# Kernel optimization log

Measured on AMD Instinct MI355X. Metric: run time of the kernel, lower is better.

Reference implementation:

```python
import jax, jax.numpy as jnp
import numpy as np

D_MODEL = 1024
SCALE = 1.0 / np.sqrt(D_MODEL)


def setup_inputs() -> dict:
    key = jax.random.key(0)
    ks = jax.random.split(key, 9)
    B, S, D = 4, 2048, D_MODEL
    std = 1.0 / np.sqrt(D)
    x = jax.random.normal(ks[0], (B, S, D), dtype=jnp.float32)
    # nn.Linear weights: [out, in]; we store transposed [in, out] for x @ W
    Wq = jax.random.uniform(ks[1], (D, D), jnp.float32, -std, std)
    bq = jax.random.uniform(ks[2], (D,), jnp.float32, -std, std)
    Wk = jax.random.uniform(ks[3], (D, D), jnp.float32, -std, std)
    bk = jax.random.uniform(ks[4], (D,), jnp.float32, -std, std)
    Wv = jax.random.uniform(ks[5], (D, D), jnp.float32, -std, std)
    bv = jax.random.uniform(ks[6], (D,), jnp.float32, -std, std)
    Wo = jax.random.uniform(ks[7], (D, D), jnp.float32, -std, std)
    bo = jax.random.uniform(ks[8], (D,), jnp.float32, -std, std)
    return {"x": x, "Wq": Wq, "bq": bq, "Wk": Wk, "bk": bk,
            "Wv": Wv, "bv": bv, "Wo": Wo, "bo": bo}


def reference(x, Wq, bq, Wk, bk, Wv, bv, Wo, bo):
    q = x @ Wq + bq                      # [B,S,D]
    k = x @ Wk + bk
    v = x @ Wv + bv
    scores = jnp.einsum('bsd,btd->bst', q, k) * SCALE  # [B,S,S]
    weights = jax.nn.softmax(scores, axis=-1)
    out = jnp.einsum('bst,btd->bsd', weights, v)       # [B,S,D]
    return out @ Wo + bo
```

## Files before the change

kernel.cpp:

```cpp
#include <hip/hip_runtime.h>
#include <hip/hip_bf16.h>
#include <cstdint>

typedef __bf16 bf16x8 __attribute__((ext_vector_type(8)));
typedef float f32x4 __attribute__((ext_vector_type(4)));

__device__ __forceinline__ float bf2f(unsigned short u) {
  union { unsigned int i; float f; } x; x.i = ((unsigned int)u) << 16; return x.f;
}
__device__ __forceinline__ unsigned short f2bf(float f) {
  __hip_bfloat16 h = __float2bfloat16(f);
  return __builtin_bit_cast(unsigned short, h);
}

__device__ __forceinline__ void gload_lds16(const void* g, void* l) {
  auto gp = reinterpret_cast<__attribute__((address_space(1))) char*>(
      reinterpret_cast<uintptr_t>(g));
  auto lp = reinterpret_cast<__attribute__((address_space(3))) char*>(
      reinterpret_cast<uintptr_t>(l));
  __builtin_amdgcn_global_load_lds(gp, lp, 16, 0, 0);
}

__device__ __forceinline__ void xcd_swz(int& bx, int& by, int& bz) {
  const int gx = gridDim.x, gy = gridDim.y;
  const int n = gx * gy * (int)gridDim.z;
  int lin = blockIdx.x + gx * (blockIdx.y + gy * blockIdx.z);
  lin = (lin & 7) * (n >> 3) + (lin >> 3);
  bx = lin % gx; lin /= gx;
  by = lin % gy; bz = lin / gy;
}

__global__ __launch_bounds__(256) void cvt_f32_to_bf16(
    const float* __restrict__ in, unsigned short* __restrict__ out, long n4) {
  long i = (long)blockIdx.x * 256 + threadIdx.x;
  if (i >= n4) return;
  const float4 v = reinterpret_cast<const float4*>(in)[i];
  ushort4 o;
  o.x = f2bf(v.x); o.y = f2bf(v.y); o.z = f2bf(v.z); o.w = f2bf(v.w);
  reinterpret_cast<ushort4*>(out)[i] = o;
}

__global__ void transpose_w4(const float* __restrict__ w0,
                             const float* __restrict__ w1,
                             const float* __restrict__ w2,
                             const float* __restrict__ w3,
                             unsigned short* __restrict__ out) {
  const int z = blockIdx.z;
  const float* in = (z == 0) ? w0 : (z == 1) ? w1 : (z == 2) ? w2 : w3;
  out += (size_t)z * 1024 * 1024;
  __shared__ float tile[32][33];
  const int c0 = blockIdx.x * 32, r0 = blockIdx.y * 32;
  tile[threadIdx.y][threadIdx.x] =
      in[(size_t)(r0 + threadIdx.y) * 1024 + c0 + threadIdx.x];
  __syncthreads();
  out[(size_t)(c0 + threadIdx.y) * 1024 + r0 + threadIdx.x] =
      f2bf(tile[threadIdx.x][threadIdx.y]);
}

__global__ void concat_bias3(const float* a, const float* b, const float* c,
                             float* o) {
  int i = blockIdx.x * 256 + threadIdx.x;
  if (i >= 3072) return;
  o[i] = (i < 1024) ? a[i] : (i < 2048 ? b[i - 1024] : c[i - 2048]);
}

template <typename OutT, bool HAS_BIAS, bool VSPLIT>
__global__ __launch_bounds__(256, 4) void gemm_hi(
    const unsigned short* __restrict__ A,
    const unsigned short* __restrict__ Bt,
    OutT* __restrict__ C,
    const float* __restrict__ bias,
    unsigned short* __restrict__ vt,
    int K, int lda, int ldb, int ldc, float scale,
    long sA, long sB, long sC) {
  int bx, by, bz;
  xcd_swz(bx, by, bz);
  A  += (long)bz * sA;
  Bt += (long)bz * sB;
  C  += (long)bz * sC;
  const int n0 = bx << 7;
  const int m0 = by << 7;
  __shared__ __attribute__((aligned(16))) unsigned short As[128 * 64];
  __shared__ __attribute__((aligned(16))) unsigned short Bs[128 * 64];
  const int t = threadIdx.x;
  const int lane = t & 63;
  const int w = t >> 6;
  const int wm = w >> 1, wn = w & 1;
  const unsigned short* gA = A + (size_t)m0 * lda;
  const unsigned short* gB = Bt + (size_t)n0 * ldb;
  const int NT = K >> 6;

  const int srow = lane >> 3;
  const int scol = ((lane & 7) ^ srow) << 3;

  f32x4 acc[4][4];
  const f32x4 vz = {0.f, 0.f, 0.f, 0.f};
#pragma unroll
  for (int i = 0; i < 4; ++i)
#pragma unroll
    for (int j = 0; j < 4; ++j) acc[i][j] = vz;

  for (int kt = 0; kt < NT; ++kt) {
    const unsigned short* pA = gA + (size_t)kt * 64;
    const unsigned short* pB = gB + (size_t)kt * 64;
#pragma unroll
    for (int i = 0; i < 4; ++i) {
      const int r0 = (w << 3) + (i << 5);
      gload_lds16(pA + (size_t)(r0 + srow) * lda + scol, As + r0 * 64);
      gload_lds16(pB + (size_t)(r0 + srow) * ldb + scol, Bs + r0 * 64);
    }
    __syncthreads();

#pragma unroll
    for (int kk = 0; kk < 2; ++kk) {
      bf16x8 af[4], bg[4];
      const int ch = ((kk << 2) + (lane >> 4)) ^ (lane & 7);
#pragma unroll
      for (int m = 0; m < 4; ++m) {
        const int row = (wm << 6) + (m << 4) + (lane & 15);
        af[m] = *reinterpret_cast<const bf16x8*>(As + row * 64 + (ch << 3));
      }
#pragma unroll
      for (int n = 0; n < 4; ++n) {
        const int row = (wn << 6) + (n << 4) + (lane & 15);
        bg[n] = *reinterpret_cast<const bf16x8*>(Bs + row * 64 + (ch << 3));
      }
#pragma unroll
      for (int m = 0; m < 4; ++m)
#pragma unroll
        for (int n = 0; n < 4; ++n) {
          if constexpr (VSPLIT) {
            acc[m][n] = __builtin_amdgcn_mfma_f32_16x16x32_bf16(
                af[m], bg[n], acc[m][n], 0, 0, 0);
          } else {
            acc[m][n] = __builtin_amdgcn_mfma_f32_16x16x32_bf16(
                bg[n], af[m], acc[m][n], 0, 0, 0);
          }
        }
    }
    __syncthreads();
  }

  if constexpr (VSPLIT) {
    const int crow0 = m0 + (wm << 6) + ((lane >> 4) << 2);
    const int ccol0 = n0 + (wn << 6) + (lane & 15);
    if (n0 >= 2048) {
      const int b = m0 >> 11;
#pragma unroll
      for (int mf = 0; mf < 4; ++mf) {
#pragma unroll
        for (int nf = 0; nf < 4; ++nf) {
          const int col = ccol0 + (nf << 4);
          const float bb = HAS_BIAS ? bias[col] : 0.f;
          const int d = col - 2048;
          const int s = (crow0 & 2047) + (mf << 4);
          ushort4 o;
          o.x = f2bf(acc[mf][nf][0] * scale + bb);
          o.y = f2bf(acc[mf][nf][1] * scale + bb);
          o.z = f2bf(acc[mf][nf][2] * scale + bb);
          o.w = f2bf(acc[mf][nf][3] * scale + bb);
          *reinterpret_cast<ushort4*>(
              vt + (((size_t)b << 10) + d) * 2048 + s) = o;
        }
      }
    } else {
#pragma unroll
      for (int mf = 0; mf < 4; ++mf) {
#pragma unroll
        for (int nf = 0; nf < 4; ++nf) {
          const int col = ccol0 + (nf << 4);
          const float bb = HAS_BIAS ? bias[col] : 0.f;
#pragma unroll
          for (int i = 0; i < 4; ++i) {
            const int row = crow0 + (mf << 4) + i;
            C[(size_t)row * ldc + col] =
                (OutT)f2bf(acc[mf][nf][i] * scale + bb);
          }
        }
      }
    }
  } else {
    const int mrow0 = m0 + (wm << 6) + (lane & 15);
    const int ncol0 = n0 + (wn << 6) + ((lane >> 4) << 2);
#pragma unroll
    for (int mf = 0; mf < 4; ++mf) {
      const int row = mrow0 + (mf << 4);
#pragma unroll
      for (int nf = 0; nf < 4; ++nf) {
        const int col = ncol0 + (nf << 4);
        float4 bb = {0.f, 0.f, 0.f, 0.f};
        if (HAS_BIAS) bb = *reinterpret_cast<const float4*>(bias + col);
        const f32x4 a = acc[mf][nf];
        if constexpr (sizeof(OutT) == 2) {
          ushort4 o;
          o.x = f2bf(a[0] * scale + bb.x);
          o.y = f2bf(a[1] * scale + bb.y);
          o.z = f2bf(a[2] * scale + bb.z);
          o.w = f2bf(a[3] * scale + bb.w);
          *reinterpret_cast<ushort4*>(&C[(size_t)row * ldc + col]) = o;
        } else {
          float4 o;
          o.x = a[0] * scale + bb.x;
          o.y = a[1] * scale + bb.y;
          o.z = a[2] * scale + bb.z;
          o.w = a[3] * scale + bb.w;
          *reinterpret_cast<float4*>(&C[(size_t)row * ldc + col]) = o;
        }
      }
    }
  }
}

__global__ __launch_bounds__(256) void softmax_inplace(
    unsigned short* __restrict__ P, int S) {
  const size_t row = blockIdx.x;
  unsigned short* p = P + row * (size_t)S;
  const int t = threadIdx.x;
  const int lane = t & 63, w = t >> 6;
  const uint4 raw = reinterpret_cast<const uint4*>(p)[t];
  unsigned int u[4] = {raw.x, raw.y, raw.z, raw.w};
  float v[8];
#pragma unroll
  for (int j = 0; j < 4; ++j) {
    v[2 * j]     = bf2f((unsigned short)(u[j] & 0xffffu));
    v[2 * j + 1] = bf2f((unsigned short)(u[j] >> 16));
  }
  float mx = v[0];
#pragma unroll
  for (int j = 1; j < 8; ++j) mx = fmaxf(mx, v[j]);
#pragma unroll
  for (int off = 32; off >= 1; off >>= 1) mx = fmaxf(mx, __shfl_xor(mx, off, 64));
  __shared__ float red[4];
  if (lane == 0) red[w] = mx;
  __syncthreads();
  mx = fmaxf(fmaxf(red[0], red[1]), fmaxf(red[2], red[3]));
  float e[8];
  float s = 0.f;
#pragma unroll
  for (int j = 0; j < 8; ++j) { e[j] = __expf(v[j] - mx); s += e[j]; }
#pragma unroll
  for (int off = 32; off >= 1; off >>= 1) s += __shfl_xor(s, off, 64);
  __syncthreads();
  if (lane == 0) red[w] = s;
  __syncthreads();
  s = red[0] + red[1] + red[2] + red[3];
  const float inv = 1.f / s;
  unsigned int o[4];
#pragma unroll
  for (int j = 0; j < 4; ++j)
    o[j] = (unsigned int)f2bf(e[2 * j] * inv) |
           ((unsigned int)f2bf(e[2 * j + 1] * inv) << 16);
  uint4 ov; ov.x = o[0]; ov.y = o[1]; ov.z = o[2]; ov.w = o[3];
  reinterpret_cast<uint4*>(p)[t] = ov;
}

extern "C" void kernel_launch(void* const* d_in, const int* in_sizes, int n_in,
                              void* d_out, int out_size, void* d_ws, size_t ws_size,
                              hipStream_t stream) {
  (void)in_sizes; (void)n_in; (void)out_size; (void)ws_size;
  const float* x  = (const float*)d_in[0];
  const float* Wq = (const float*)d_in[1];
  const float* bq = (const float*)d_in[2];
  const float* Wk = (const float*)d_in[3];
  const float* bk = (const float*)d_in[4];
  const float* Wv = (const float*)d_in[5];
  const float* bv = (const float*)d_in[6];
  const float* Wo = (const float*)d_in[7];
  const float* bo = (const float*)d_in[8];
  float* out = (float*)d_out;

  constexpr int B = 4, S = 2048, D = 1024;
  constexpr long BS = (long)B * S;
  constexpr size_t MB = 1ull << 20;
  char* ws = (char*)d_ws;
  unsigned short* xb   = (unsigned short*)(ws + 0);
  unsigned short* Wall = (unsigned short*)(ws + 16 * MB);
  float*          bqkv = (float*)(ws + 24 * MB);
  unsigned short* QKVc = (unsigned short*)(ws + 25 * MB);
  unsigned short* Vt   = (unsigned short*)(ws + 57 * MB);
  unsigned short* Sc   = (unsigned short*)(ws + 73 * MB);
  unsigned short* AO   = (unsigned short*)(ws + 0);

  const float scale = 0.03125f;

  cvt_f32_to_bf16<<<(BS * D / 4 + 255) / 256, 256, 0, stream>>>(x, xb, BS * D / 4);
  transpose_w4<<<dim3(32, 32, 4), dim3(32, 32), 0, stream>>>(Wq, Wk, Wv, Wo, Wall);
  concat_bias3<<<12, 256, 0, stream>>>(bq, bk, bv, bqkv);

  gemm_hi<unsigned short, true, true><<<dim3(24, 64, 1), 256, 0, stream>>>(
      xb, Wall, QKVc, bqkv, Vt, D, D, D, 2048, 1.f, 0, 0, 0);

  gemm_hi<unsigned short, false, false><<<dim3(16, 16, 4), 256, 0, stream>>>(
      QKVc + 0, QKVc + 1024, Sc, nullptr, nullptr, D, 2048, 2048, S, scale,
      (long)S * 2048, (long)S * 2048, (long)S * S);

  softmax_inplace<<<B * S, 256, 0, stream>>>(Sc, S);

  gemm_hi<unsigned short, false, false><<<dim3(8, 16, 4), 256, 0, stream>>>(
      Sc, Vt, AO, nullptr, nullptr, S, S, S, D, 1.f,
      (long)S * S, (long)D * S, (long)S * D);

  gemm_hi<float, true, false><<<dim3(8, 64, 1), 256, 0, stream>>>(
      AO, Wall + 3 * 1024 * 1024, out, bo, nullptr, D, D, D, D, 1.f, 0, 0, 0);
}
```

Measured before the change: 207.6 us.

## Fuse input conversion into QKV GEMM and softmax into PV GEMM

```diff
diff --git a/kernel.cpp b/kernel.cpp
--- a/kernel.cpp
+++ b/kernel.cpp
@@ -4,6 +4,7 @@
 
 typedef __bf16 bf16x8 __attribute__((ext_vector_type(8)));
 typedef float f32x4 __attribute__((ext_vector_type(4)));
+typedef short short8 __attribute__((ext_vector_type(8)));
 
 __device__ __forceinline__ float bf2f(unsigned short u) {
   union { unsigned int i; float f; } x; x.i = ((unsigned int)u) << 16; return x.f;
@@ -28,16 +29,6 @@
   lin = (lin & 7) * (n >> 3) + (lin >> 3);
   bx = lin % gx; lin /= gx;
   by = lin % gy; bz = lin / gy;
-}
-
-__global__ __launch_bounds__(256) void cvt_f32_to_bf16(
-    const float* __restrict__ in, unsigned short* __restrict__ out, long n4) {
-  long i = (long)blockIdx.x * 256 + threadIdx.x;
-  if (i >= n4) return;
-  const float4 v = reinterpret_cast<const float4*>(in)[i];
-  ushort4 o;
-  o.x = f2bf(v.x); o.y = f2bf(v.y); o.z = f2bf(v.z); o.w = f2bf(v.w);
-  reinterpret_cast<ushort4*>(out)[i] = o;
 }
 
 __global__ void transpose_w4(const float* __restrict__ w0,
@@ -64,13 +55,120 @@
   o[i] = (i < 1024) ? a[i] : (i < 2048 ? b[i - 1024] : c[i - 2048]);
 }
 
-template <typename OutT, bool HAS_BIAS, bool VSPLIT>
+__global__ __launch_bounds__(256, 4) void gemm_qkv(
+    const float* __restrict__ xf,
+    const unsigned short* __restrict__ Bt,
+    unsigned short* __restrict__ C,
+    const float* __restrict__ bias,
+    unsigned short* __restrict__ vt) {
+  int bx, by, bz;
+  xcd_swz(bx, by, bz);
+  const int n0 = bx << 7;
+  const int m0 = by << 7;
+  __shared__ __attribute__((aligned(16))) unsigned short As[128 * 64];
+  __shared__ __attribute__((aligned(16))) unsigned short Bs[128 * 64];
+  const int t = threadIdx.x;
+  const int lane = t & 63;
+  const int w = t >> 6;
+  const int wm = w >> 1, wn = w & 1;
+  const unsigned short* gB = Bt + (size_t)n0 * 1024;
+
+  const int srow = lane >> 3;
+  const int gcol8 = ((lane & 7) ^ srow) << 3;
+
+  f32x4 acc[4][4];
+  const f32x4 vz = {0.f, 0.f, 0.f, 0.f};
+#pragma unroll
+  for (int i = 0; i < 4; ++i)
+#pragma unroll
+    for (int j = 0; j < 4; ++j) acc[i][j] = vz;
+
+  for (int kt = 0; kt < 16; ++kt) {
+    const unsigned short* pB = gB + (size_t)kt * 64;
+    const float* pA = xf + (size_t)m0 * 1024 + (size_t)kt * 64;
+#pragma unroll
+    for (int i = 0; i < 4; ++i) {
+      const int r0 = (w << 3) + (i << 5);
+      gload_lds16(pB + (size_t)(r0 + srow) * 1024 + gcol8, Bs + r0 * 64);
+      const float* s = pA + (size_t)(r0 + srow) * 1024 + gcol8;
+      const float4 a0 = *reinterpret_cast<const float4*>(s);
+      const float4 a1 = *reinterpret_cast<const float4*>(s + 4);
+      short8 pk;
+      pk[0] = (short)f2bf(a0.x); pk[1] = (short)f2bf(a0.y);
+      pk[2] = (short)f2bf(a0.z); pk[3] = (short)f2bf(a0.w);
+      pk[4] = (short)f2bf(a1.x); pk[5] = (short)f2bf(a1.y);
+      pk[6] = (short)f2bf(a1.z); pk[7] = (short)f2bf(a1.w);
+      *reinterpret_cast<short8*>(As + (r0 + srow) * 64 + ((lane & 7) << 3)) = pk;
+    }
+    __syncthreads();
+
+#pragma unroll
+    for (int kk = 0; kk < 2; ++kk) {
+      bf16x8 af[4], bg[4];
+      const int ch = ((kk << 2) + (lane >> 4)) ^ (lane & 7);
+#pragma unroll
+      for (int m = 0; m < 4; ++m) {
+        const int row = (wm << 6) + (m << 4) + (lane & 15);
+        af[m] = *reinterpret_cast<const bf16x8*>(As + row * 64 + (ch << 3));
+      }
+#pragma unroll
+      for (int n = 0; n < 4; ++n) {
+        const int row = (wn << 6) + (n << 4) + (lane & 15);
+        bg[n] = *reinterpret_cast<const bf16x8*>(Bs + row * 64 + (ch << 3));
+      }
+#pragma unroll
+      for (int m = 0; m < 4; ++m)
+#pragma unroll
+        for (int n = 0; n < 4; ++n)
+          acc[m][n] = __builtin_amdgcn_mfma_f32_16x16x32_bf16(
+              af[m], bg[n], acc[m][n], 0, 0, 0);
+    }
+    __syncthreads();
+  }
+
+  const int crow0 = m0 + (wm << 6) + ((lane >> 4) << 2);
+  const int ccol0 = n0 + (wn << 6) + (lane & 15);
+  if (n0 >= 2048) {
+    const int b = m0 >> 11;
+#pragma unroll
+    for (int mf = 0; mf < 4; ++mf) {
+#pragma unroll
+      for (int nf = 0; nf < 4; ++nf) {
+        const int col = ccol0 + (nf << 4);
+        const float bb = bias[col];
+        const int d = col - 2048;
+        const int s = (crow0 & 2047) + (mf << 4);
+        ushort4 o;
+        o.x = f2bf(acc[mf][nf][0] + bb);
+        o.y = f2bf(acc[mf][nf][1] + bb);
+        o.z = f2bf(acc[mf][nf][2] + bb);
+        o.w = f2bf(acc[mf][nf][3] + bb);
+        *reinterpret_cast<ushort4*>(vt + (((size_t)b << 10) + d) * 2048 + s) = o;
+      }
+    }
+  } else {
+#pragma unroll
+    for (int mf = 0; mf < 4; ++mf) {
+#pragma unroll
+      for (int nf = 0; nf < 4; ++nf) {
+        const int col = ccol0 + (nf << 4);
+        const float bb = bias[col];
+#pragma unroll
+        for (int i = 0; i < 4; ++i) {
+          const int row = crow0 + (mf << 4) + i;
+          C[(size_t)row * 2048 + col] = f2bf(acc[mf][nf][i] + bb);
+        }
+      }
+    }
+  }
+}
+
+template <typename OutT, bool HAS_BIAS>
 __global__ __launch_bounds__(256, 4) void gemm_hi(
     const unsigned short* __restrict__ A,
     const unsigned short* __restrict__ Bt,
     OutT* __restrict__ C,
     const float* __restrict__ bias,
-    unsigned short* __restrict__ vt,
     int K, int lda, int ldb, int ldc, float scale,
     long sA, long sB, long sC) {
   int bx, by, bz;
@@ -128,130 +226,157 @@
 #pragma unroll
       for (int m = 0; m < 4; ++m)
 #pragma unroll
-        for (int n = 0; n < 4; ++n) {
-          if constexpr (VSPLIT) {
-            acc[m][n] = __builtin_amdgcn_mfma_f32_16x16x32_bf16(
-                af[m], bg[n], acc[m][n], 0, 0, 0);
-          } else {
-            acc[m][n] = __builtin_amdgcn_mfma_f32_16x16x32_bf16(
-                bg[n], af[m], acc[m][n], 0, 0, 0);
-          }
-        }
-    }
-    __syncthreads();
-  }
-
-  if constexpr (VSPLIT) {
-    const int crow0 = m0 + (wm << 6) + ((lane >> 4) << 2);
-    const int ccol0 = n0 + (wn << 6) + (lane & 15);
-    if (n0 >= 2048) {
-      const int b = m0 >> 11;
-#pragma unroll
-      for (int mf = 0; mf < 4; ++mf) {
-#pragma unroll
-        for (int nf = 0; nf < 4; ++nf) {
-          const int col = ccol0 + (nf << 4);
-          const float bb = HAS_BIAS ? bias[col] : 0.f;
-          const int d = col - 2048;
-          const int s = (crow0 & 2047) + (mf << 4);
-          ushort4 o;
-          o.x = f2bf(acc[mf][nf][0] * scale + bb);
-          o.y = f2bf(acc[mf][nf][1] * scale + bb);
-          o.z = f2bf(acc[mf][nf][2] * scale + bb);
-          o.w = f2bf(acc[mf][nf][3] * scale + bb);
-          *reinterpret_cast<ushort4*>(
-              vt + (((size_t)b << 10) + d) * 2048 + s) = o;
-        }
-      }
-    } else {
-#pragma unroll
-      for (int mf = 0; mf < 4; ++mf) {
-#pragma unroll
-        for (int nf = 0; nf < 4; ++nf) {
-          const int col = ccol0 + (nf << 4);
-          const float bb = HAS_BIAS ? bias[col] : 0.f;
-#pragma unroll
-          for (int i = 0; i < 4; ++i) {
-            const int row = crow0 + (mf << 4) + i;
-            C[(size_t)row * ldc + col] =
-                (OutT)f2bf(acc[mf][nf][i] * scale + bb);
-          }
-        }
-      }
-    }
-  } else {
-    const int mrow0 = m0 + (wm << 6) + (lane & 15);
-    const int ncol0 = n0 + (wn << 6) + ((lane >> 4) << 2);
+        for (int n = 0; n < 4; ++n)
+          acc[m][n] = __builtin_amdgcn_mfma_f32_16x16x32_bf16(
+              bg[n], af[m], acc[m][n], 0, 0, 0);
+    }
+    __syncthreads();
+  }
+
+  const int mrow0 = m0 + (wm << 6) + (lane & 15);
+  const int ncol0 = n0 + (wn << 6) + ((lane >> 4) << 2);
+#pragma unroll
+  for (int mf = 0; mf < 4; ++mf) {
+    const int row = mrow0 + (mf << 4);
+#pragma unroll
+    for (int nf = 0; nf < 4; ++nf) {
+      const int col = ncol0 + (nf << 4);
+      float4 bb = {0.f, 0.f, 0.f, 0.f};
+      if (HAS_BIAS) bb = *reinterpret_cast<const float4*>(bias + col);
+      const f32x4 a = acc[mf][nf];
+      if constexpr (sizeof(OutT) == 2) {
+        ushort4 o;
+        o.x = f2bf(a[0] * scale + bb.x);
+        o.y = f2bf(a[1] * scale + bb.y);
+        o.z = f2bf(a[2] * scale + bb.z);
+        o.w = f2bf(a[3] * scale + bb.w);
+        *reinterpret_cast<ushort4*>(&C[(size_t)row * ldc + col]) = o;
+      } else {
+        float4 o;
+        o.x = a[0] * scale + bb.x;
+        o.y = a[1] * scale + bb.y;
+        o.z = a[2] * scale + bb.z;
+        o.w = a[3] * scale + bb.w;
+        *reinterpret_cast<float4*>(&C[(size_t)row * ldc + col]) = o;
+      }
+    }
+  }
+}
+
+__global__ __launch_bounds__(256, 3) void gemm_pv(
+    const unsigned short* __restrict__ Sc,
+    const unsigned short* __restrict__ Vt,
+    unsigned short* __restrict__ O) {
+  int bx, by, bz;
+  xcd_swz(bx, by, bz);
+  const unsigned short* P = Sc + (long)bz * 2048 * 2048;
+  const unsigned short* V = Vt + (long)bz * 1024 * 2048;
+  unsigned short* Ob = O + (long)bz * 2048 * 1024;
+  const int n0 = bx << 7;
+  const int m0 = by << 7;
+  __shared__ __attribute__((aligned(16))) unsigned short Bs[128 * 64];
+  const int t = threadIdx.x;
+  const int lane = t & 63;
+  const int w = t >> 6;
+  const int wm = w >> 1, wn = w & 1;
+  const int srow = lane >> 3;
+  const int scol = ((lane & 7) ^ srow) << 3;
+  const int chh = lane >> 4;
+
+  f32x4 acc[4][4];
+  const f32x4 vz = {0.f, 0.f, 0.f, 0.f};
+#pragma unroll
+  for (int i = 0; i < 4; ++i)
+#pragma unroll
+    for (int j = 0; j < 4; ++j) acc[i][j] = vz;
+  float mrun[4] = {-1e30f, -1e30f, -1e30f, -1e30f};
+  float lpart[4] = {0.f, 0.f, 0.f, 0.f};
+
+  for (int kt = 0; kt < 32; ++kt) {
+    const unsigned short* pV = V + (size_t)kt * 64;
+#pragma unroll
+    for (int i = 0; i < 4; ++i) {
+      const int r0 = (w << 3) + (i << 5);
+      gload_lds16(pV + (size_t)(n0 + r0 + srow) * 2048 + scol, Bs + r0 * 64);
+    }
+
+    bf16x8 af[4][2];
 #pragma unroll
     for (int mf = 0; mf < 4; ++mf) {
-      const int row = mrow0 + (mf << 4);
+      const int row = m0 + (wm << 6) + (mf << 4) + (lane & 15);
+      const unsigned short* pr = P + (size_t)row * 2048 + kt * 64;
+      const bf16x8 r0v = *reinterpret_cast<const bf16x8*>(pr + (chh << 3));
+      const bf16x8 r1v = *reinterpret_cast<const bf16x8*>(pr + 32 + (chh << 3));
+      float f[16];
+#pragma unroll
+      for (int j = 0; j < 8; ++j) { f[j] = (float)r0v[j]; f[8 + j] = (float)r1v[j]; }
+      float px = f[0];
+#pragma unroll
+      for (int j = 1; j < 16; ++j) px = fmaxf(px, f[j]);
+      px = fmaxf(px, __shfl_xor(px, 16, 64));
+      px = fmaxf(px, __shfl_xor(px, 32, 64));
+      const float mn = fmaxf(mrun[mf], px);
+      const float sc = __expf(mrun[mf] - mn);
+      mrun[mf] = mn;
+      float ls = 0.f;
+#pragma unroll
+      for (int j = 0; j < 16; ++j) { f[j] = __expf(f[j] - mn); ls += f[j]; }
+      lpart[mf] = lpart[mf] * sc + ls;
 #pragma unroll
       for (int nf = 0; nf < 4; ++nf) {
-        const int col = ncol0 + (nf << 4);
-        float4 bb = {0.f, 0.f, 0.f, 0.f};
-        if (HAS_BIAS) bb = *reinterpret_cast<const float4*>(bias + col);
-        const f32x4 a = acc[mf][nf];
-        if constexpr (sizeof(OutT) == 2) {
-          ushort4 o;
-          o.x = f2bf(a[0] * scale + bb.x);
-          o.y = f2bf(a[1] * scale + bb.y);
-          o.z = f2bf(a[2] * scale + bb.z);
-          o.w = f2bf(a[3] * scale + bb.w);
-          *reinterpret_cast<ushort4*>(&C[(size_t)row * ldc + col]) = o;
-        } else {
-          float4 o;
-          o.x = a[0] * scale + bb.x;
-          o.y = a[1] * scale + bb.y;
-          o.z = a[2] * scale + bb.z;
-          o.w = a[3] * scale + bb.w;
-          *reinterpret_cast<float4*>(&C[(size_t)row * ldc + col]) = o;
-        }
-      }
-    }
-  }
-}
-
-__global__ __launch_bounds__(256) void softmax_inplace(
-    unsigned short* __restrict__ P, int S) {
-  const size_t row = blockIdx.x;
-  unsigned short* p = P + row * (size_t)S;
-  const int t = threadIdx.x;
-  const int lane = t & 63, w = t >> 6;
-  const uint4 raw = reinterpret_cast<const uint4*>(p)[t];
-  unsigned int u[4] = {raw.x, raw.y, raw.z, raw.w};
-  float v[8];
-#pragma unroll
-  for (int j = 0; j < 4; ++j) {
-    v[2 * j]     = bf2f((unsigned short)(u[j] & 0xffffu));
-    v[2 * j + 1] = bf2f((unsigned short)(u[j] >> 16));
-  }
-  float mx = v[0];
-#pragma unroll
-  for (int j = 1; j < 8; ++j) mx = fmaxf(mx, v[j]);
-#pragma unroll
-  for (int off = 32; off >= 1; off >>= 1) mx = fmaxf(mx, __shfl_xor(mx, off, 64));
-  __shared__ float red[4];
-  if (lane == 0) red[w] = mx;
-  __syncthreads();
-  mx = fmaxf(fmaxf(red[0], red[1]), fmaxf(red[2], red[3]));
-  float e[8];
-  float s = 0.f;
-#pragma unroll
-  for (int j = 0; j < 8; ++j) { e[j] = __expf(v[j] - mx); s += e[j]; }
-#pragma unroll
-  for (int off = 32; off >= 1; off >>= 1) s += __shfl_xor(s, off, 64);
-  __syncthreads();
-  if (lane == 0) red[w] = s;
-  __syncthreads();
-  s = red[0] + red[1] + red[2] + red[3];
-  const float inv = 1.f / s;
-  unsigned int o[4];
-#pragma unroll
-  for (int j = 0; j < 4; ++j)
-    o[j] = (unsigned int)f2bf(e[2 * j] * inv) |
-           ((unsigned int)f2bf(e[2 * j + 1] * inv) << 16);
-  uint4 ov; ov.x = o[0]; ov.y = o[1]; ov.z = o[2]; ov.w = o[3];
-  reinterpret_cast<uint4*>(p)[t] = ov;
+        acc[mf][nf][0] *= sc; acc[mf][nf][1] *= sc;
+        acc[mf][nf][2] *= sc; acc[mf][nf][3] *= sc;
+      }
+      short8 p0, p1;
+#pragma unroll
+      for (int j = 0; j < 8; ++j) {
+        p0[j] = (short)f2bf(f[j]);
+        p1[j] = (short)f2bf(f[8 + j]);
+      }
+      af[mf][0] = __builtin_bit_cast(bf16x8, p0);
+      af[mf][1] = __builtin_bit_cast(bf16x8, p1);
+    }
+
+    __syncthreads();
+#pragma unroll
+    for (int kk = 0; kk < 2; ++kk) {
+      bf16x8 bg[4];
+      const int ch = ((kk << 2) + chh) ^ (lane & 7);
+#pragma unroll
+      for (int n = 0; n < 4; ++n) {
+        const int row = (wn << 6) + (n << 4) + (lane & 15);
+        bg[n] = *reinterpret_cast<const bf16x8*>(Bs + row * 64 + (ch << 3));
+      }
+#pragma unroll
+      for (int m = 0; m < 4; ++m)
+#pragma unroll
+        for (int n = 0; n < 4; ++n)
+          acc[m][n] = __builtin_amdgcn_mfma_f32_16x16x32_bf16(
+              bg[n], af[m][kk], acc[m][n], 0, 0, 0);
+    }
+    __syncthreads();
+  }
+
+  const int mrow0 = m0 + (wm << 6) + (lane & 15);
+  const int ncol0 = n0 + (wn << 6) + (chh << 2);
+#pragma unroll
+  for (int mf = 0; mf < 4; ++mf) {
+    float l = lpart[mf];
+    l += __shfl_xor(l, 16, 64);
+    l += __shfl_xor(l, 32, 64);
+    const float inv = 1.f / l;
+    const int row = mrow0 + (mf << 4);
+#pragma unroll
+    for (int nf = 0; nf < 4; ++nf) {
+      const int col = ncol0 + (nf << 4);
+      ushort4 o;
+      o.x = f2bf(acc[mf][nf][0] * inv);
+      o.y = f2bf(acc[mf][nf][1] * inv);
+      o.z = f2bf(acc[mf][nf][2] * inv);
+      o.w = f2bf(acc[mf][nf][3] * inv);
+      *reinterpret_cast<ushort4*>(&Ob[(size_t)row * 1024 + col]) = o;
+    }
+  }
 }
 
 extern "C" void kernel_launch(void* const* d_in, const int* in_sizes, int n_in,
@@ -270,36 +395,28 @@
   float* out = (float*)d_out;
 
   constexpr int B = 4, S = 2048, D = 1024;
-  constexpr long BS = (long)B * S;
   constexpr size_t MB = 1ull << 20;
   char* ws = (char*)d_ws;
-  unsigned short* xb   = (unsigned short*)(ws + 0);
-  unsigned short* Wall = (unsigned short*)(ws + 16 * MB);
-  float*          bqkv = (float*)(ws + 24 * MB);
-  unsigned short* QKVc = (unsigned short*)(ws + 25 * MB);
-  unsigned short* Vt   = (unsigned short*)(ws + 57 * MB);
-  unsigned short* Sc   = (unsigned short*)(ws + 73 * MB);
-  unsigned short* AO   = (unsigned short*)(ws + 0);
+  unsigned short* Wall = (unsigned short*)(ws + 0);
+  float*          bqkv = (float*)(ws + 8 * MB);
+  unsigned short* QKVc = (unsigned short*)(ws + 9 * MB);
+  unsigned short* Vt   = (unsigned short*)(ws + 41 * MB);
+  unsigned short* Sc   = (unsigned short*)(ws + 57 * MB);
+  unsigned short* AO   = (unsigned short*)(ws + 89 * MB);
 
   const float scale = 0.03125f;
 
-  cvt_f32_to_bf16<<<(BS * D / 4 + 255) / 256, 256, 0, stream>>>(x, xb, BS * D / 4);
   transpose_w4<<<dim3(32, 32, 4), dim3(32, 32), 0, stream>>>(Wq, Wk, Wv, Wo, Wall);
   concat_bias3<<<12, 256, 0, stream>>>(bq, bk, bv, bqkv);
 
-  gemm_hi<unsigned short, true, true><<<dim3(24, 64, 1), 256, 0, stream>>>(
-      xb, Wall, QKVc, bqkv, Vt, D, D, D, 2048, 1.f, 0, 0, 0);
-
-  gemm_hi<unsigned short, false, false><<<dim3(16, 16, 4), 256, 0, stream>>>(
-      QKVc + 0, QKVc + 1024, Sc, nullptr, nullptr, D, 2048, 2048, S, scale,
+  gemm_qkv<<<dim3(24, 64, 1), 256, 0, stream>>>(x, Wall, QKVc, bqkv, Vt);
+
+  gemm_hi<unsigned short, false><<<dim3(16, 16, 4), 256, 0, stream>>>(
+      QKVc + 0, QKVc + 1024, Sc, nullptr, D, 2048, 2048, S, scale,
       (long)S * 2048, (long)S * 2048, (long)S * S);
 
-  softmax_inplace<<<B * S, 256, 0, stream>>>(Sc, S);
-
-  gemm_hi<unsigned short, false, false><<<dim3(8, 16, 4), 256, 0, stream>>>(
-      Sc, Vt, AO, nullptr, nullptr, S, S, S, D, 1.f,
-      (long)S * S, (long)D * S, (long)S * D);
-
-  gemm_hi<float, true, false><<<dim3(8, 64, 1), 256, 0, stream>>>(
-      AO, Wall + 3 * 1024 * 1024, out, bo, nullptr, D, D, D, D, 1.f, 0, 0, 0);
-}
+  gemm_pv<<<dim3(8, 16, 4), 256, 0, stream>>>(Sc, Vt, AO);
+
+  gemm_hi<float, true><<<dim3(8, 64, 1), 256, 0, stream>>>(
+      AO, Wall + 3 * 1024 * 1024, out, bo, D, D, D, D, 1.f, 0, 0, 0);
+}
```

Measured after the change: 289.6 us. 1.4x slower.
